# Optimization experiments

Hardware: AMD Instinct MI355X
Metric: run time of the kernel (lower is better)

The kernel has to match this reference:

```python
import jax, jax.numpy as jnp
import numpy as np

WIDTHS = list(range(5, 50, 5))    # 9 widths
SIGMAS = list(range(2, 22, 2))    # 10 sigmas -> 90 filters
KMAX = 45                          # pad all kernels to max width
SUB_LOW_RATIO = 1.0
TOPK = 64


def _build_kernels():
    # Normalized 1D Gaussian kernels, zero-padded to KMAX and centered.
    # Zero taps contribute nothing, so SAME-padded conv matches per-width conv.
    ks = []
    for w in WIDTHS:
        for s in SIGMAS:
            x = np.arange(w, dtype=np.float32) - (w - 1) / 2.0
            g = np.exp(-x * x / (2.0 * s * s)).astype(np.float32)
            g /= g.sum()
            pad = np.zeros(KMAX, np.float32)
            off = (KMAX - w) // 2
            pad[off:off + w] = g
            ks.append(pad)
    return jnp.asarray(np.stack(ks))  # [90, KMAX]


def setup_inputs() -> dict:
    key = jax.random.key(0)
    k1, k2, k3 = jax.random.split(key, 3)
    return {
        "image": jax.random.normal(k1, (4, 3, 256, 256), jnp.float32),
        "kernels": _build_kernels(),                                   # fixed Gaussian buffers
        "channel_prompt": jax.random.normal(k2, (90,), jnp.float32),   # learned gating
        "lambda_param": jax.random.normal(k3, (1,), jnp.float32) * 0.1,
    }


def _hfc_all(image, kernels):
    # image: [B,C,H,W]; kernels: [F,K]. Returns high-pass stack [F,B,C,H,W].
    B, C, H, W = image.shape
    F = kernels.shape[0]
    x = image.reshape(B * C, 1, H, W)
    kv = kernels.reshape(F, 1, KMAX, 1)   # vertical pass (per-channel -> F filters)
    kh = kernels.reshape(F, 1, 1, KMAX)   # horizontal pass (depthwise over F)
    dn = ('NCHW', 'OIHW', 'NCHW')
    y = jax.lax.conv_general_dilated(x, kv, (1, 1), 'SAME', dimension_numbers=dn)
    low = jax.lax.conv_general_dilated(y, kh, (1, 1), 'SAME',
                                       feature_group_count=F, dimension_numbers=dn)
    low = low.reshape(B, C, F, H, W).transpose(2, 0, 1, 3, 4)  # [F,B,C,H,W]
    # high-frequency component, clamped (is_clamp=True)
    return jnp.clip(image[None] - SUB_LOW_RATIO * low, -1.0, 1.0)


def reference(image, kernels, channel_prompt, lambda_param):
    lam = jax.nn.sigmoid(lambda_param)[0]
    hfc = _hfc_all(image, kernels)                 # [90,B,C,H,W]
    _, idx = jax.lax.top_k(channel_prompt, TOPK)   # select 64 experts
    top = hfc[idx]                                 # gather [64,B,C,H,W]
    # pairwise lambda mixup -> [32,B,C,H,W] (stacked list of mixed images)
    mixed = lam * top[0::2] + (1.0 - lam) * top[1::2]
    return mixed
```

## Files before the change

### kernel.cpp

```cpp
#include <hip/hip_runtime.h>
#include <hip/hip_bf16.h>
#include <math.h>

typedef __attribute__((ext_vector_type(8))) short bf16x8;
typedef __attribute__((ext_vector_type(4))) float f32x4;

#define HST2 80
#define PLANE_STRIDE 92416
#define ROW_STRIDE   304

#define WS_IDX   0
#define WS_LAM   256
#define WS_FRAG  4096
#define WS_IMG   266240

#define NB_PREP 542

__device__ __forceinline__ unsigned f2bf(float f) {
    unsigned u = __builtin_bit_cast(unsigned, f);
    u += 0x7FFFu + ((u >> 16) & 1u);
    return u >> 16;
}

__device__ __forceinline__ unsigned pk2(float a, float b) {
    return f2bf(a) | (f2bf(b) << 16);
}

__global__ __launch_bounds__(128) void gmix_topk(const float* __restrict__ cp,
                                                 const float* __restrict__ lp,
                                                 int* __restrict__ idx,
                                                 float* __restrict__ lam) {
    int i = threadIdx.x;
    if (i < 90) {
        float v = cp[i];
        int rank = 0;
        for (int j = 0; j < 90; ++j) {
            float vj = cp[j];
            rank += (vj > v) || (vj == v && j < i);
        }
        if (rank < 64) idx[rank] = i;
    }
    if (i == 0) lam[0] = 1.0f / (1.0f + expf(-lp[0]));
}

__global__ __launch_bounds__(256) void gmix_prep(const float* __restrict__ img,
                                                 const float* __restrict__ kers,
                                                 const int* __restrict__ idx,
                                                 short* __restrict__ wsimg,
                                                 short* __restrict__ frag) {
    const int b   = blockIdx.x;
    const int tid = threadIdx.x;
    if (b < NB_PREP) {
        const int cid = b * 256 + tid;
        if (cid >= 12 * 304 * 38) return;
        const int plane = cid / (304 * 38);
        const int rr    = cid % (304 * 38);
        const int r     = rr / 38;
        const int ch    = rr % 38;
        uint4 o = {0u, 0u, 0u, 0u};
        const int gr = r - 22;
        if (gr >= 0 && gr < 256 && ch >= 3 && ch < 35) {
            const float* sp = img + (size_t)plane * 65536 + gr * 256 + (ch * 8 - 24);
            const float4 v0 = *(const float4*)sp;
            const float4 v1 = *(const float4*)(sp + 4);
            o.x = pk2(v0.x, v0.y);
            o.y = pk2(v0.z, v0.w);
            o.z = pk2(v1.x, v1.y);
            o.w = pk2(v1.z, v1.w);
        }
        *(uint4*)(wsimg + plane * PLANE_STRIDE + r * ROW_STRIDE + ch * 8) = o;
    } else if (tid < 64) {
        const int unit  = b - NB_PREP;
        const int fid   = unit >> 1;
        const int v     = unit & 1;
        const int f     = idx[fid];
        const int lm    = tid & 15;
        const int lg    = tid >> 4;
        const int shift = v ? 0 : 2;
        short* dst = frag + ((size_t)unit * 64 + tid) * 16;
#pragma unroll
        for (int ka = 0; ka < 2; ++ka)
#pragma unroll
            for (int e = 0; e < 8; ++e) {
                const int k = ka * 32 + lg * 8 + e;
                const int d = k - lm - shift;
                const float t = (d >= 0 && d < 45) ? kers[f * 45 + d] : 0.f;
                dst[ka * 8 + e] = (short)f2bf(t);
            }
    }
}

__global__ __launch_bounds__(512, 2) void gmix_mfma(const float* __restrict__ img,
                                                    const short* __restrict__ wsimg,
                                                    const short* __restrict__ frag,
                                                    const float* __restrict__ lamp,
                                                    float* __restrict__ out) {
    __shared__ short HT[2][128 * HST2];

    const int tid  = threadIdx.x;
    const int lane = tid & 63;
    const int wv   = tid >> 6;
    const int lm   = lane & 15;
    const int lg   = lane >> 4;

    const int bid   = blockIdx.x;
    const int pg    = bid / 192;
    const int rem   = bid % 192;
    const int plane = rem >> 4;
    const int band  = (rem >> 1) & 7;
    const int half  = rem & 1;
    const int r0    = band * 32;

    const float* imgp = img + (size_t)plane * 65536;
    const float  lam  = lamp[0];

    const short* abase = wsimg + plane * PLANE_STRIDE + (r0 + lm) * ROW_STRIDE
                       + half * 128 + wv * 16 + lg * 8;
    bf16x8 a0s[5], a1s[5];
#pragma unroll
    for (int t1 = 0; t1 < 5; ++t1) {
        a0s[t1] = *(const bf16x8*)(abase + t1 * 16 * ROW_STRIDE);
        a1s[t1] = *(const bf16x8*)(abase + t1 * 16 * ROW_STRIDE + 32);
    }

    const int ocol = half * 128 + wv * 16 + lg * 4;
    f32x4 ivs[2];
#pragma unroll
    for (int t = 0; t < 2; ++t)
        ivs[t] = *(const f32x4*)(imgp + (r0 + t * 16 + lm) * 256 + ocol);

    short*       htw = &HT[0][(wv * 16 + lm) * HST2 + lg * 4];
    const short* htr = &HT[0][(wv * 16 + lm) * HST2 + lg * 8];
    const int    FOF = 128 * HST2;

#pragma unroll 1
    for (int i = 0; i < 4; ++i) {
        const int p = pg * 4 + i;

        const short* fbA = frag + (size_t)(2 * p) * 2048;
        const short* fbB = fbA + 2048;
        const bf16x8 bA1_0 = *(const bf16x8*)(fbA + lane * 16);
        const bf16x8 bA1_1 = *(const bf16x8*)(fbA + lane * 16 + 8);
        const bf16x8 bA2_0 = *(const bf16x8*)(fbA + 1024 + lane * 16);
        const bf16x8 bA2_1 = *(const bf16x8*)(fbA + 1024 + lane * 16 + 8);
        const bf16x8 bB1_0 = *(const bf16x8*)(fbB + lane * 16);
        const bf16x8 bB1_1 = *(const bf16x8*)(fbB + lane * 16 + 8);
        const bf16x8 bB2_0 = *(const bf16x8*)(fbB + 1024 + lane * 16);
        const bf16x8 bB2_1 = *(const bf16x8*)(fbB + 1024 + lane * 16 + 8);

#pragma unroll
        for (int t1 = 0; t1 < 5; ++t1) {
            f32x4 accA = {0.f, 0.f, 0.f, 0.f};
            f32x4 accB = {0.f, 0.f, 0.f, 0.f};
            accA = __builtin_amdgcn_mfma_f32_16x16x32_bf16(a0s[t1], bA1_0, accA, 0, 0, 0);
            accB = __builtin_amdgcn_mfma_f32_16x16x32_bf16(a0s[t1], bB1_0, accB, 0, 0, 0);
            accA = __builtin_amdgcn_mfma_f32_16x16x32_bf16(a1s[t1], bA1_1, accA, 0, 0, 0);
            accB = __builtin_amdgcn_mfma_f32_16x16x32_bf16(a1s[t1], bB1_1, accB, 0, 0, 0);
            uint2 pkA, pkB;
            pkA.x = pk2(accA[0], accA[1]);
            pkA.y = pk2(accA[2], accA[3]);
            pkB.x = pk2(accB[0], accB[1]);
            pkB.y = pk2(accB[2], accB[3]);
            *(uint2*)(htw + t1 * 16) = pkA;
            *(uint2*)(htw + FOF + t1 * 16) = pkB;
        }

        float* outp = out + ((size_t)(p * 12 + plane) << 16);
#pragma unroll
        for (int t = 0; t < 2; ++t) {
            const bf16x8 hA0 = *(const bf16x8*)(htr + t * 16);
            const bf16x8 hA1 = *(const bf16x8*)(htr + t * 16 + 32);
            const bf16x8 hB0 = *(const bf16x8*)(htr + FOF + t * 16);
            const bf16x8 hB1 = *(const bf16x8*)(htr + FOF + t * 16 + 32);
            f32x4 aA = {0.f, 0.f, 0.f, 0.f};
            f32x4 aB = {0.f, 0.f, 0.f, 0.f};
            aA = __builtin_amdgcn_mfma_f32_16x16x32_bf16(hA0, bA2_0, aA, 0, 0, 0);
            aB = __builtin_amdgcn_mfma_f32_16x16x32_bf16(hB0, bB2_0, aB, 0, 0, 0);
            aA = __builtin_amdgcn_mfma_f32_16x16x32_bf16(hA1, bA2_1, aA, 0, 0, 0);
            aB = __builtin_amdgcn_mfma_f32_16x16x32_bf16(hB1, bB2_1, aB, 0, 0, 0);

            f32x4 res;
#pragma unroll
            for (int q = 0; q < 4; ++q) {
                float hA = ivs[t][q] - aA[q];
                hA = fminf(fmaxf(hA, -1.f), 1.f);
                float hB = ivs[t][q] - aB[q];
                hB = fminf(fmaxf(hB, -1.f), 1.f);
                res[q] = lam * hA + (1.0f - lam) * hB;
            }
            *(f32x4*)(outp + (r0 + t * 16 + lm) * 256 + ocol) = res;
        }
    }
}

extern "C" void kernel_launch(void* const* d_in, const int* in_sizes, int n_in,
                              void* d_out, int out_size, void* d_ws, size_t ws_size,
                              hipStream_t stream) {
    const float* image   = (const float*)d_in[0];
    const float* kernels = (const float*)d_in[1];
    const float* prompt  = (const float*)d_in[2];
    const float* lambdap = (const float*)d_in[3];
    float* out = (float*)d_out;

    int*   ws_idx  = (int*)d_ws;
    float* ws_lam  = (float*)((char*)d_ws + WS_LAM);
    short* ws_frag = (short*)((char*)d_ws + WS_FRAG);
    short* ws_img  = (short*)((char*)d_ws + WS_IMG);

    gmix_topk<<<1, 128, 0, stream>>>(prompt, lambdap, ws_idx, ws_lam);
    gmix_prep<<<NB_PREP + 128, 256, 0, stream>>>(image, kernels, ws_idx, ws_img, ws_frag);
    gmix_mfma<<<1536, 512, 0, stream>>>(image, ws_img, ws_frag, ws_lam, out);
}
```

Measured before the change: 57.27 us.

## Fuse top-k into prep kernel and retile MFMA blocks to 64x64 squares

Removes the separate top-k launch: each filter-prep block now ranks the prompt itself into shared memory, and the sigmoid of lambda is computed inline in the main kernel. The main kernel switches from 32x128 tiles with 512 threads to 64x64 tiles with 256 threads and four blocks per CU. A-operand loads move into the vertical loop instead of being preloaded. Square tiles cut the vertical-halo overhead per output (7 row tiles per 4 instead of 5 per 2), and dropping a launch saves launch latency. The cost is redundant top-k work in 128 blocks and more LDS per output row.

```diff
diff --git a/kernel.cpp b/kernel.cpp
--- a/kernel.cpp
+++ b/kernel.cpp
@@ -5,14 +5,13 @@
 typedef __attribute__((ext_vector_type(8))) short bf16x8;
 typedef __attribute__((ext_vector_type(4))) float f32x4;
 
-#define HST2 80
+#define HST3 120
+#define FOF  (64 * HST3)
 #define PLANE_STRIDE 92416
 #define ROW_STRIDE   304
 
-#define WS_IDX   0
-#define WS_LAM   256
-#define WS_FRAG  4096
-#define WS_IMG   266240
+#define WS_FRAG 0
+#define WS_IMG  262144
 
 #define NB_PREP 542
 
@@ -26,28 +25,12 @@
     return f2bf(a) | (f2bf(b) << 16);
 }
 
-__global__ __launch_bounds__(128) void gmix_topk(const float* __restrict__ cp,
-                                                 const float* __restrict__ lp,
-                                                 int* __restrict__ idx,
-                                                 float* __restrict__ lam) {
-    int i = threadIdx.x;
-    if (i < 90) {
-        float v = cp[i];
-        int rank = 0;
-        for (int j = 0; j < 90; ++j) {
-            float vj = cp[j];
-            rank += (vj > v) || (vj == v && j < i);
-        }
-        if (rank < 64) idx[rank] = i;
-    }
-    if (i == 0) lam[0] = 1.0f / (1.0f + expf(-lp[0]));
-}
-
 __global__ __launch_bounds__(256) void gmix_prep(const float* __restrict__ img,
                                                  const float* __restrict__ kers,
-                                                 const int* __restrict__ idx,
+                                                 const float* __restrict__ cp,
                                                  short* __restrict__ wsimg,
                                                  short* __restrict__ frag) {
+    __shared__ int smap[64];
     const int b   = blockIdx.x;
     const int tid = threadIdx.x;
     if (b < NB_PREP) {
@@ -69,33 +52,45 @@
             o.w = pk2(v1.z, v1.w);
         }
         *(uint4*)(wsimg + plane * PLANE_STRIDE + r * ROW_STRIDE + ch * 8) = o;
-    } else if (tid < 64) {
-        const int unit  = b - NB_PREP;
-        const int fid   = unit >> 1;
-        const int v     = unit & 1;
-        const int f     = idx[fid];
-        const int lm    = tid & 15;
-        const int lg    = tid >> 4;
-        const int shift = v ? 0 : 2;
-        short* dst = frag + ((size_t)unit * 64 + tid) * 16;
-#pragma unroll
-        for (int ka = 0; ka < 2; ++ka)
-#pragma unroll
-            for (int e = 0; e < 8; ++e) {
-                const int k = ka * 32 + lg * 8 + e;
-                const int d = k - lm - shift;
-                const float t = (d >= 0 && d < 45) ? kers[f * 45 + d] : 0.f;
-                dst[ka * 8 + e] = (short)f2bf(t);
+    } else {
+        if (tid < 90) {
+            const float mv = cp[tid];
+            int rank = 0;
+            for (int j = 0; j < 90; ++j) {
+                const float vj = cp[j];
+                rank += (vj > mv) || (vj == mv && j < tid);
             }
+            if (rank < 64) smap[rank] = tid;
+        }
+        __syncthreads();
+        if (tid < 64) {
+            const int unit  = b - NB_PREP;
+            const int fid   = unit >> 1;
+            const int v     = unit & 1;
+            const int f     = smap[fid];
+            const int lm    = tid & 15;
+            const int lg    = tid >> 4;
+            const int shift = v ? 0 : 2;
+            short* dst = frag + ((size_t)unit * 64 + tid) * 16;
+#pragma unroll
+            for (int ka = 0; ka < 2; ++ka)
+#pragma unroll
+                for (int e = 0; e < 8; ++e) {
+                    const int k = ka * 32 + lg * 8 + e;
+                    const int d = k - lm - shift;
+                    const float t = (d >= 0 && d < 45) ? kers[f * 45 + d] : 0.f;
+                    dst[ka * 8 + e] = (short)f2bf(t);
+                }
+        }
     }
 }
 
-__global__ __launch_bounds__(512, 2) void gmix_mfma(const float* __restrict__ img,
+__global__ __launch_bounds__(256, 4) void gmix_mfma(const float* __restrict__ img,
                                                     const short* __restrict__ wsimg,
                                                     const short* __restrict__ frag,
-                                                    const float* __restrict__ lamp,
+                                                    const float* __restrict__ lp,
                                                     float* __restrict__ out) {
-    __shared__ short HT[2][128 * HST2];
+    __shared__ short HT[2 * 64 * HST3];
 
     const int tid  = threadIdx.x;
     const int lane = tid & 63;
@@ -107,31 +102,25 @@
     const int pg    = bid / 192;
     const int rem   = bid % 192;
     const int plane = rem >> 4;
-    const int band  = (rem >> 1) & 7;
-    const int half  = rem & 1;
-    const int r0    = band * 32;
+    const int band  = (rem >> 2) & 3;
+    const int qcol  = rem & 3;
+    const int r0    = band * 64;
+    const int c0    = qcol * 64;
 
     const float* imgp = img + (size_t)plane * 65536;
-    const float  lam  = lamp[0];
+    const float  lam  = 1.f / (1.f + expf(-lp[0]));
+
+    const int ocol = c0 + wv * 16 + lg * 4;
+    f32x4 ivs[4];
+#pragma unroll
+    for (int t = 0; t < 4; ++t)
+        ivs[t] = *(const f32x4*)(imgp + (r0 + t * 16 + lm) * 256 + ocol);
 
     const short* abase = wsimg + plane * PLANE_STRIDE + (r0 + lm) * ROW_STRIDE
-                       + half * 128 + wv * 16 + lg * 8;
-    bf16x8 a0s[5], a1s[5];
-#pragma unroll
-    for (int t1 = 0; t1 < 5; ++t1) {
-        a0s[t1] = *(const bf16x8*)(abase + t1 * 16 * ROW_STRIDE);
-        a1s[t1] = *(const bf16x8*)(abase + t1 * 16 * ROW_STRIDE + 32);
-    }
-
-    const int ocol = half * 128 + wv * 16 + lg * 4;
-    f32x4 ivs[2];
-#pragma unroll
-    for (int t = 0; t < 2; ++t)
-        ivs[t] = *(const f32x4*)(imgp + (r0 + t * 16 + lm) * 256 + ocol);
-
-    short*       htw = &HT[0][(wv * 16 + lm) * HST2 + lg * 4];
-    const short* htr = &HT[0][(wv * 16 + lm) * HST2 + lg * 8];
-    const int    FOF = 128 * HST2;
+                       + c0 + wv * 16 + lg * 8;
+
+    short*       htw = &HT[(wv * 16 + lm) * HST3 + lg * 4];
+    const short* htr = &HT[(wv * 16 + lm) * HST3 + lg * 8];
 
 #pragma unroll 1
     for (int i = 0; i < 4; ++i) {
@@ -149,13 +138,15 @@
         const bf16x8 bB2_1 = *(const bf16x8*)(fbB + 1024 + lane * 16 + 8);
 
 #pragma unroll
-        for (int t1 = 0; t1 < 5; ++t1) {
+        for (int t1 = 0; t1 < 7; ++t1) {
+            const bf16x8 a0 = *(const bf16x8*)(abase + t1 * 16 * ROW_STRIDE);
+            const bf16x8 a1 = *(const bf16x8*)(abase + t1 * 16 * ROW_STRIDE + 32);
             f32x4 accA = {0.f, 0.f, 0.f, 0.f};
             f32x4 accB = {0.f, 0.f, 0.f, 0.f};
-            accA = __builtin_amdgcn_mfma_f32_16x16x32_bf16(a0s[t1], bA1_0, accA, 0, 0, 0);
-            accB = __builtin_amdgcn_mfma_f32_16x16x32_bf16(a0s[t1], bB1_0, accB, 0, 0, 0);
-            accA = __builtin_amdgcn_mfma_f32_16x16x32_bf16(a1s[t1], bA1_1, accA, 0, 0, 0);
-            accB = __builtin_amdgcn_mfma_f32_16x16x32_bf16(a1s[t1], bB1_1, accB, 0, 0, 0);
+            accA = __builtin_amdgcn_mfma_f32_16x16x32_bf16(a0, bA1_0, accA, 0, 0, 0);
+            accB = __builtin_amdgcn_mfma_f32_16x16x32_bf16(a0, bB1_0, accB, 0, 0, 0);
+            accA = __builtin_amdgcn_mfma_f32_16x16x32_bf16(a1, bA1_1, accA, 0, 0, 0);
+            accB = __builtin_amdgcn_mfma_f32_16x16x32_bf16(a1, bB1_1, accB, 0, 0, 0);
             uint2 pkA, pkB;
             pkA.x = pk2(accA[0], accA[1]);
             pkA.y = pk2(accA[2], accA[3]);
@@ -167,7 +158,7 @@
 
         float* outp = out + ((size_t)(p * 12 + plane) << 16);
 #pragma unroll
-        for (int t = 0; t < 2; ++t) {
+        for (int t = 0; t < 4; ++t) {
             const bf16x8 hA0 = *(const bf16x8*)(htr + t * 16);
             const bf16x8 hA1 = *(const bf16x8*)(htr + t * 16 + 32);
             const bf16x8 hB0 = *(const bf16x8*)(htr + FOF + t * 16);
@@ -202,12 +193,9 @@
     const float* lambdap = (const float*)d_in[3];
     float* out = (float*)d_out;
 
-    int*   ws_idx  = (int*)d_ws;
-    float* ws_lam  = (float*)((char*)d_ws + WS_LAM);
     short* ws_frag = (short*)((char*)d_ws + WS_FRAG);
     short* ws_img  = (short*)((char*)d_ws + WS_IMG);
 
-    gmix_topk<<<1, 128, 0, stream>>>(prompt, lambdap, ws_idx, ws_lam);
-    gmix_prep<<<NB_PREP + 128, 256, 0, stream>>>(image, kernels, ws_idx, ws_img, ws_frag);
-    gmix_mfma<<<1536, 512, 0, stream>>>(image, ws_img, ws_frag, ws_lam, out);
-}
+    gmix_prep<<<NB_PREP + 128, 256, 0, stream>>>(image, kernels, prompt, ws_img, ws_frag);
+    gmix_mfma<<<1536, 256, 0, stream>>>(image, ws_img, ws_frag, lambdap, out);
+}
```

Measured after the change: 48.88 us. 1.17x faster.
